# Performance work log

Hardware: AMD Instinct MI355X
Metric: run time of the kernel (lower is better)

## Reference

```python
import jax, jax.numpy as jnp
from jax import lax
import numpy as np

N_LOOP, N_LAYER, FS = 2, 10, 2
RES_CH, DIL_CH, SKIP_CH, COND_DIM = 64, 128, 128, 80
DILATIONS = [2 ** i for i in range(N_LAYER)] * N_LOOP  # 20 layers
L = len(DILATIONS)
B, T = 4, 8192


def setup_inputs() -> dict:
    key = jax.random.key(0)
    ks = jax.random.split(key, 10)
    s = 0.05
    return {
        "x": jax.random.normal(ks[0], (B, RES_CH, T, 1), jnp.float32),
        "condition": jax.random.normal(ks[1], (B, COND_DIM, T, 1), jnp.float32),
        # stacked per-layer params (L layers)
        "conv_w": jax.random.normal(ks[2], (L, DIL_CH, RES_CH, FS), jnp.float32) * s,
        "conv_b": jax.random.normal(ks[3], (L, DIL_CH), jnp.float32) * s,
        "cond_w": jax.random.normal(ks[4], (L, DIL_CH, COND_DIM), jnp.float32) * s,
        "cond_b": jax.random.normal(ks[5], (L, DIL_CH), jnp.float32) * s,
        "res_w": jax.random.normal(ks[6], (L, RES_CH, DIL_CH // 2), jnp.float32) * s,
        "res_b": jax.random.normal(ks[7], (L, RES_CH), jnp.float32) * s,
        "skip_w": jax.random.normal(ks[8], (L, SKIP_CH, DIL_CH // 2), jnp.float32) * s,
        "skip_b": jax.random.normal(ks[9], (L, SKIP_CH), jnp.float32) * s,
    }


def reference(x, condition, conv_w, conv_b, cond_w, cond_b, res_w, res_b, skip_w, skip_b):
    # Drop trailing width-1 dim: [B,C,T,1] -> [B,C,T]
    xs = x[..., 0]
    cond = condition[..., 0]
    skip_total = None
    for i, d in enumerate(DILATIONS):
        # torch pads d*(FS-1) on both sides then crops [:T] == left-only causal pad
        h = lax.conv_general_dilated(
            xs, conv_w[i], window_strides=(1,),
            padding=[(d * (FS - 1), 0)], rhs_dilation=(d,),
            dimension_numbers=("NCH", "OIH", "NCH"),
        ) + conv_b[i][None, :, None]
        # 1x1 condition projection, broadcast add
        h = h + jnp.einsum("ch,bht->bct", cond_w[i], cond) + cond_b[i][None, :, None]
        tanh_z, sig_z = jnp.split(h, 2, axis=1)
        z = jnp.tanh(tanh_z) * jax.nn.sigmoid(sig_z)  # [B, DIL_CH//2, T]
        xs = jnp.einsum("oc,bct->bot", res_w[i], z) + res_b[i][None, :, None] + xs
        skip = jnp.einsum("oc,bct->bot", skip_w[i], z) + skip_b[i][None, :, None]
        skip_total = skip if skip_total is None else skip_total + skip
    return skip_total[..., None]  # [B, SKIP_CH, T, 1]
```

## Files before the change

### kernel.cpp

```cpp
#include <hip/hip_runtime.h>

#define BATCH 4
#define TLEN 8192
#define NLAYER 20
#define NTILE 128
#define GUARD 8
#define ATILE (NTILE + GUARD)
#define CELL 4096

typedef __attribute__((ext_vector_type(8))) short bf16x8;
typedef __attribute__((ext_vector_type(8))) unsigned short u16x8;
typedef __attribute__((ext_vector_type(4))) short s16x4;
typedef __attribute__((ext_vector_type(4))) float f32x4;

__device__ __forceinline__ unsigned short f2b(float f) {
    unsigned u = __float_as_uint(f);
    return (unsigned short)((u + 0x7fffu + ((u >> 16) & 1u)) >> 16);
}
__device__ __forceinline__ unsigned cvtpk(float lo, float hi) {
    unsigned r;
    asm("v_cvt_pk_bf16_f32 %0, %1, %2" : "=v"(r) : "v"(lo), "v"(hi));
    return r;
}

__global__ void prep_w(const float* __restrict__ conv_w, const float* __restrict__ conv_b,
                       const float* __restrict__ cond_w, const float* __restrict__ cond_b,
                       const float* __restrict__ res_w,  const float* __restrict__ res_b,
                       const float* __restrict__ skip_w, const float* __restrict__ skip_b,
                       unsigned short* __restrict__ w1f, unsigned short* __restrict__ w2f,
                       unsigned short* __restrict__ wsf,
                       float* __restrict__ hb, float* __restrict__ rb, float* __restrict__ sbt) {
    const int l = blockIdx.x, tid = threadIdx.x;
    const int start = blockIdx.y * 256 + tid;
    for (int idx = start; idx < 7 * 8 * 512; idx += 2048) {
        int ks = idx >> 12;
        int slot = (idx >> 9) & 7, lane = (idx >> 3) & 63, j = idx & 7;
        int m = (slot & 1) * 64 + (slot >> 1) * 16 + (lane & 15);
        int k = ks * 32 + ((lane >> 4) << 3) + j;
        float v;
        if (k < 64)       v = conv_w[(((size_t)l * 128 + m) * 64 + k) * 2 + 0];
        else if (k < 128) v = conv_w[(((size_t)l * 128 + m) * 64 + (k - 64)) * 2 + 1];
        else if (k < 208) v = cond_w[((size_t)l * 128 + m) * 80 + (k - 128)];
        else              v = 0.0f;
        w1f[(size_t)l * 7 * 8 * 512 + idx] = f2b(v);
    }
    for (int idx = start; idx < 2 * 4 * 512; idx += 2048) {
        int ks = idx >> 11;
        int slot = (idx >> 9) & 3, lane = (idx >> 3) & 63, j = idx & 7;
        int m = slot * 16 + (lane & 15);
        int k = ks * 32 + ((lane >> 4) << 3) + j;
        w2f[(size_t)l * 2 * 4 * 512 + idx] = f2b(res_w[((size_t)l * 64 + m) * 64 + k]);
    }
    for (int idx = start; idx < 2 * 8 * 512; idx += 2048) {
        int ks = idx >> 12;
        int slot = (idx >> 9) & 7, lane = (idx >> 3) & 63, j = idx & 7;
        int m = slot * 16 + (lane & 15);
        int k = ks * 32 + ((lane >> 4) << 3) + j;
        wsf[(size_t)l * 2 * 8 * 512 + idx] = f2b(skip_w[((size_t)l * 128 + m) * 64 + k]);
    }
    if (blockIdx.y == 0) {
        if (tid < 128) hb[l * 128 + tid] = conv_b[l * 128 + tid] + cond_b[l * 128 + tid];
        if (tid < 64)  rb[l * 64 + tid] = res_b[l * 64 + tid];
        if (l == 0 && tid < 128) {
            float s = 0.f;
            for (int q = 0; q < NLAYER; ++q) s += skip_b[q * 128 + tid];
            sbt[tid] = s;
        }
    }
}

__global__ void prep_xc(const float* __restrict__ x, const float* __restrict__ cond,
                        unsigned short* __restrict__ xall, unsigned short* __restrict__ condc,
                        unsigned* __restrict__ flags) {
    const int tile = blockIdx.x, b = blockIdx.y, tid = threadIdx.x;
    if (tile < GUARD) {
        s16x4 zh = {0, 0, 0, 0};
        for (int s = 0; s < NLAYER; ++s) {
            unsigned short* g = xall + ((size_t)s * BATCH + b) * ATILE * CELL + (size_t)tile * CELL;
            for (int idx = tid * 4; idx < CELL; idx += 1024)
                *(s16x4*)(g + idx) = zh;
        }
        if (tile == 0)
            for (int i = tid; i < NTILE * 32; i += 256)
                flags[(size_t)b * NTILE * 32 + i] = 0u;
        return;
    }
    __shared__ float xt[64][64];
    __shared__ float ct[80][64];
    const int rt = tile - GUARD;
    for (int idx = tid; idx < 64 * 64; idx += 256) {
        int ch = idx >> 6, n = idx & 63;
        xt[ch][n] = x[((size_t)b * 64 + ch) * TLEN + rt * 64 + n];
    }
    for (int idx = tid; idx < 80 * 64; idx += 256) {
        int ch = idx >> 6, n = idx & 63;
        ct[ch][n] = cond[((size_t)b * 80 + ch) * TLEN + rt * 64 + n];
    }
    __syncthreads();
    unsigned short* s0 = xall + ((size_t)b * ATILE + tile) * CELL;
    for (int idx = tid; idx < 8 * 64; idx += 256) {
        int cg = idx >> 6, n = idx & 63;
        unsigned short* dbf = s0 + ((size_t)cg * 64 + n) * 8;
        #pragma unroll
        for (int j = 0; j < 8; ++j) dbf[j] = f2b(xt[cg * 8 + j][n]);
    }
    for (int idx = tid; idx < 12 * 64; idx += 256) {
        int cg = idx >> 6, n = idx & 63;
        u16x8 cell;
        #pragma unroll
        for (int j = 0; j < 8; ++j) {
            int ch = cg * 8 + j;
            cell[j] = (ch < 80) ? f2b(ct[ch][n]) : (unsigned short)0;
        }
        *(u16x8*)(condc + (((size_t)(b * NTILE + rt) * 12 + cg) * 64 + n) * 8) = cell;
    }
}

__global__ __launch_bounds__(256, 2) void wavenet_fused(
    const float* __restrict__ x, const unsigned short* __restrict__ condc,
    unsigned short* __restrict__ xall,
    const unsigned short* __restrict__ w1f, const unsigned short* __restrict__ w2f,
    const unsigned short* __restrict__ wsf,
    const float* __restrict__ hb, const float* __restrict__ rb,
    const float* __restrict__ sbt, float* __restrict__ out,
    unsigned* __restrict__ flags) {
    __shared__ unsigned short s_cond[12 * 512];
    __shared__ unsigned short s_xc[CELL];
    __shared__ unsigned short s_zc[CELL];

    const int b = blockIdx.y, tile = blockIdx.x, t0 = tile * 64;
    const int tid = threadIdx.x, lane = tid & 63;
    const int wv = __builtin_amdgcn_readfirstlane(tid >> 6);
    const int ln = lane & 15, lg = lane >> 4;
    const int r0 = wv * 16 + lg * 4;
    const int cgz = r0 >> 3, j0z = r0 & 7;
    const size_t bslot = (size_t)BATCH * ATILE * CELL;

    {
        const u16x8* cc = (const u16x8*)(condc + (size_t)(b * NTILE + tile) * 12 * 512);
        u16x8* sc = (u16x8*)s_cond;
        for (int i = tid; i < 768; i += 256) sc[i] = cc[i];
        const u16x8* xc = (const u16x8*)(xall + ((size_t)b * ATILE + tile + GUARD) * CELL);
        u16x8* sx = (u16x8*)s_xc;
        for (int i = tid; i < 512; i += 256) sx[i] = xc[i];
    }

    f32x4 xsr[4];
    #pragma unroll
    for (int nf = 0; nf < 4; ++nf)
        #pragma unroll
        for (int r = 0; r < 4; ++r)
            xsr[nf][r] = x[((size_t)b * 64 + r0 + r) * TLEN + t0 + nf * 16 + ln];

    f32x4 skacc[2][4];
    #pragma unroll
    for (int mf = 0; mf < 2; ++mf)
        #pragma unroll
        for (int nf = 0; nf < 4; ++nf) skacc[mf][nf] = (f32x4){0.f, 0.f, 0.f, 0.f};

    unsigned fc1 = 0, fc2 = 0, fc4 = 0, fc8 = 0;
    unsigned* myflag = flags + ((size_t)b * NTILE + tile) * 32 + wv;

    __syncthreads();

    for (int l = 0; l < NLAYER; ++l) {
        const int dil = 1 << ((l < 10) ? l : (l - 10));

        if (l > 0) {
            __syncthreads();
            const int kd = (dil + 63) >> 6;
            const int tp = tile - kd;
            if (tp >= 0) {
                unsigned cached = (kd == 1) ? fc1 : (kd == 2) ? fc2 : (kd == 4) ? fc4 : fc8;
                if (cached < (unsigned)l) {
                    const unsigned* fp = flags + ((size_t)b * NTILE + tp) * 32 + (lane & 3);
                    unsigned v;
                    for (;;) {
                        v = __hip_atomic_load(fp, __ATOMIC_RELAXED, __HIP_MEMORY_SCOPE_AGENT);
                        unsigned v1 = (unsigned)__shfl_xor((int)v, 1);
                        v = (v1 < v) ? v1 : v;
                        unsigned v2 = (unsigned)__shfl_xor((int)v, 2);
                        v = (v2 < v) ? v2 : v;
                        if (v >= (unsigned)l) break;
                        __builtin_amdgcn_s_sleep(2);
                    }
                    if (kd == 1) fc1 = v; else if (kd == 2) fc2 = v;
                    else if (kd == 4) fc4 = v; else fc8 = v;
                }
            }
            __builtin_amdgcn_sched_barrier(0);
        }

        const unsigned short* xrb = xall + (size_t)l * bslot + (size_t)b * ATILE * CELL;
        const unsigned short* w1l = w1f + (size_t)l * 7 * 8 * 512;

        bf16x8 brem[2][4];
        #pragma unroll
        for (int ks = 0; ks < 2; ++ks) {
            const int cg = ks * 4 + lg;
            #pragma unroll
            for (int nf = 0; nf < 4; ++nf) {
                int u = t0 + nf * 16 + ln - dil + GUARD * 64;
                brem[ks][nf] = *(const bf16x8*)(xrb + (((size_t)(u >> 6) * 8 + cg) * 64 + (u & 63)) * 8);
            }
        }
        bf16x8 raf[4];
        raf[0] = *(const bf16x8*)(w1l + (size_t)(0 * 8 + wv * 2 + 0) * 512 + lane * 8);
        raf[1] = *(const bf16x8*)(w1l + (size_t)(0 * 8 + wv * 2 + 1) * 512 + lane * 8);
        raf[2] = *(const bf16x8*)(w1l + (size_t)(1 * 8 + wv * 2 + 0) * 512 + lane * 8);
        raf[3] = *(const bf16x8*)(w1l + (size_t)(1 * 8 + wv * 2 + 1) * 512 + lane * 8);

        f32x4 acc[2][4];
        #pragma unroll
        for (int hf = 0; hf < 2; ++hf)
            #pragma unroll
            for (int nf = 0; nf < 4; ++nf) acc[hf][nf] = (f32x4){0.f, 0.f, 0.f, 0.f};

        #pragma unroll
        for (int ks = 2; ks < 7; ++ks) {
            bf16x8 af0 = *(const bf16x8*)(w1l + (size_t)(ks * 8 + wv * 2 + 0) * 512 + lane * 8);
            bf16x8 af1 = *(const bf16x8*)(w1l + (size_t)(ks * 8 + wv * 2 + 1) * 512 + lane * 8);
            bf16x8 bfr[4];
            if (ks < 4) {
                const int cg = (ks - 2) * 4 + lg;
                #pragma unroll
                for (int nf = 0; nf < 4; ++nf)
                    bfr[nf] = *(const bf16x8*)(s_xc + ((cg * 64) + nf * 16 + ln) * 8);
            } else {
                const int cg = (ks - 4) * 4 + lg;
                #pragma unroll
                for (int nf = 0; nf < 4; ++nf)
                    bfr[nf] = *(const bf16x8*)(s_cond + ((cg * 64) + nf * 16 + ln) * 8);
            }
            #pragma unroll
            for (int nf = 0; nf < 4; ++nf) {
                acc[0][nf] = __builtin_amdgcn_mfma_f32_16x16x32_bf16(af0, bfr[nf], acc[0][nf], 0, 0, 0);
                acc[1][nf] = __builtin_amdgcn_mfma_f32_16x16x32_bf16(af1, bfr[nf], acc[1][nf], 0, 0, 0);
            }
        }

        #pragma unroll
        for (int ks = 0; ks < 2; ++ks) {
            #pragma unroll
            for (int nf = 0; nf < 4; ++nf) {
                acc[0][nf] = __builtin_amdgcn_mfma_f32_16x16x32_bf16(raf[ks * 2 + 0], brem[ks][nf], acc[0][nf], 0, 0, 0);
                acc[1][nf] = __builtin_amdgcn_mfma_f32_16x16x32_bf16(raf[ks * 2 + 1], brem[ks][nf], acc[1][nf], 0, 0, 0);
            }
        }

        {
            const float* hbl = hb + l * 128;
            float4 hbt = *(const float4*)(hbl + r0);
            float4 hbs = *(const float4*)(hbl + 64 + r0);
            #pragma unroll
            for (int nf = 0; nf < 4; ++nf) {
                float zr[4];
                #pragma unroll
                for (int r = 0; r < 4; ++r) {
                    float a  = acc[0][nf][r] + ((r == 0) ? hbt.x : (r == 1) ? hbt.y : (r == 2) ? hbt.z : hbt.w);
                    float bs = acc[1][nf][r] + ((r == 0) ? hbs.x : (r == 1) ? hbs.y : (r == 2) ? hbs.z : hbs.w);
                    float e = __expf(a + a);
                    float s = __expf(-bs);
                    zr[r] = __fdividef(e - 1.0f, (e + 1.0f) * (1.0f + s));
                }
                union { unsigned u32[2]; s16x4 v; } pk;
                pk.u32[0] = cvtpk(zr[0], zr[1]);
                pk.u32[1] = cvtpk(zr[2], zr[3]);
                *(s16x4*)(&s_zc[((cgz * 64) + nf * 16 + ln) * 8 + j0z]) = pk.v;
            }
        }
        __syncthreads();

        bf16x8 bz[2][4];
        #pragma unroll
        for (int ks = 0; ks < 2; ++ks)
            #pragma unroll
            for (int nf = 0; nf < 4; ++nf)
                bz[ks][nf] = *(const bf16x8*)(&s_zc[(((ks * 4 + lg) * 64) + nf * 16 + ln) * 8]);
        const unsigned short* wsl = wsf + (size_t)l * 2 * 8 * 512;
        bf16x8 sw[2][2];
        #pragma unroll
        for (int ks = 0; ks < 2; ++ks) {
            sw[ks][0] = *(const bf16x8*)(wsl + (size_t)(ks * 8 + wv * 2 + 0) * 512 + lane * 8);
            sw[ks][1] = *(const bf16x8*)(wsl + (size_t)(ks * 8 + wv * 2 + 1) * 512 + lane * 8);
        }

        f32x4 acc2[4];
        #pragma unroll
        for (int nf = 0; nf < 4; ++nf) acc2[nf] = (f32x4){0.f, 0.f, 0.f, 0.f};
        const unsigned short* w2l = w2f + (size_t)l * 2 * 4 * 512;
        #pragma unroll
        for (int ks = 0; ks < 2; ++ks) {
            bf16x8 a2 = *(const bf16x8*)(w2l + (size_t)(ks * 4 + wv) * 512 + lane * 8);
            #pragma unroll
            for (int nf = 0; nf < 4; ++nf)
                acc2[nf] = __builtin_amdgcn_mfma_f32_16x16x32_bf16(a2, bz[ks][nf], acc2[nf], 0, 0, 0);
        }

        {
            const float* rbl = rb + l * 64;
            float4 rbv = *(const float4*)(rbl + r0);
            unsigned short* xwt = xall + (size_t)(l + 1) * bslot +
                                  ((size_t)b * ATILE + tile + GUARD) * CELL;
            #pragma unroll
            for (int nf = 0; nf < 4; ++nf) {
                xsr[nf][0] += acc2[nf][0] + rbv.x;
                xsr[nf][1] += acc2[nf][1] + rbv.y;
                xsr[nf][2] += acc2[nf][2] + rbv.z;
                xsr[nf][3] += acc2[nf][3] + rbv.w;
                if (l < NLAYER - 1) {
                    int n = nf * 16 + ln;
                    union { unsigned u32[2]; s16x4 v; unsigned long long u64; } pk;
                    pk.u32[0] = cvtpk(xsr[nf][0], xsr[nf][1]);
                    pk.u32[1] = cvtpk(xsr[nf][2], xsr[nf][3]);
                    *(s16x4*)(&s_xc[(cgz * 64 + n) * 8 + j0z]) = pk.v;
                    __hip_atomic_store((unsigned long long*)(xwt + ((size_t)cgz * 64 + n) * 8 + j0z),
                                       pk.u64, __ATOMIC_RELAXED, __HIP_MEMORY_SCOPE_AGENT);
                }
            }
        }

        #pragma unroll
        for (int ks = 0; ks < 2; ++ks)
            #pragma unroll
            for (int nf = 0; nf < 4; ++nf) {
                skacc[0][nf] = __builtin_amdgcn_mfma_f32_16x16x32_bf16(sw[ks][0], bz[ks][nf], skacc[0][nf], 0, 0, 0);
                skacc[1][nf] = __builtin_amdgcn_mfma_f32_16x16x32_bf16(sw[ks][1], bz[ks][nf], skacc[1][nf], 0, 0, 0);
            }

        if (l < NLAYER - 1) {
            asm volatile("s_waitcnt vmcnt(0)" ::: "memory");
            if (lane == 0)
                __hip_atomic_store(myflag, (unsigned)(l + 1),
                                   __ATOMIC_RELAXED, __HIP_MEMORY_SCOPE_AGENT);
        }
    }

    #pragma unroll
    for (int mf = 0; mf < 2; ++mf)
        #pragma unroll
        for (int nf = 0; nf < 4; ++nf)
            #pragma unroll
            for (int r = 0; r < 4; ++r) {
                int m = wv * 32 + mf * 16 + lg * 4 + r;
                out[((size_t)b * 128 + m) * TLEN + t0 + nf * 16 + ln] =
                    skacc[mf][nf][r] + sbt[m];
            }
}

extern "C" void kernel_launch(void* const* d_in, const int* in_sizes, int n_in,
                              void* d_out, int out_size, void* d_ws, size_t ws_size,
                              hipStream_t stream) {
    const float* x      = (const float*)d_in[0];
    const float* cond   = (const float*)d_in[1];
    const float* conv_w = (const float*)d_in[2];
    const float* conv_b = (const float*)d_in[3];
    const float* cond_w = (const float*)d_in[4];
    const float* cond_b = (const float*)d_in[5];
    const float* res_w  = (const float*)d_in[6];
    const float* res_b  = (const float*)d_in[7];
    const float* skip_w = (const float*)d_in[8];
    const float* skip_b = (const float*)d_in[9];
    float* out = (float*)d_out;

    char* ws = (char*)d_ws;
    const size_t XALL  = (size_t)NLAYER * BATCH * ATILE * CELL * 2;
    const size_t COND  = (size_t)BATCH * NTILE * 12 * 512 * 2;
    const size_t W1    = (size_t)NLAYER * 7 * 8 * 512 * 2;
    const size_t W2    = (size_t)NLAYER * 2 * 4 * 512 * 2;
    const size_t WSF   = (size_t)NLAYER * 2 * 8 * 512 * 2;
    const size_t HB    = NLAYER * 128 * 4;
    const size_t RB    = NLAYER * 64 * 4;
    const size_t SBT   = 256 * 4;
    const size_t FLAGS = (size_t)BATCH * NTILE * 32 * 4;

    size_t off = 0;
    unsigned short* xall  = (unsigned short*)(ws + off); off += XALL;
    unsigned short* condc = (unsigned short*)(ws + off); off += COND;
    unsigned short* w1f   = (unsigned short*)(ws + off); off += W1;
    unsigned short* w2f   = (unsigned short*)(ws + off); off += W2;
    unsigned short* wsf   = (unsigned short*)(ws + off); off += WSF;
    float* hb  = (float*)(ws + off); off += HB;
    float* rb  = (float*)(ws + off); off += RB;
    float* sbt = (float*)(ws + off); off += SBT;
    unsigned* flags = (unsigned*)(ws + off); off += FLAGS;

    prep_w<<<dim3(NLAYER, 8), 256, 0, stream>>>(conv_w, conv_b, cond_w, cond_b,
                                                res_w, res_b, skip_w, skip_b,
                                                w1f, w2f, wsf, hb, rb, sbt);
    prep_xc<<<dim3(ATILE, BATCH), 256, 0, stream>>>(x, cond, xall, condc, flags);

    wavenet_fused<<<dim3(NTILE, BATCH), 256, 0, stream>>>(
        x, condc, xall, w1f, w2f, wsf, hb, rb, sbt, out, flags);
}
```

Baseline: 128.0 us.

## Merge prep kernels and precompute next layer's condition GEMM before waiting on flags

Merges the weight-prep and input-prep kernels into a single launch, removing one kernel launch and its serialization. In the fused kernel, the condition-projection part of the layer-(l+1) gate GEMM (k-slices 4..6) no longer runs at the start of that layer. It now runs right after layer l publishes its flag and before the next layer's barrier and inter-tile flag spin, so this independent MFMA work can hide the dependency wait. The cost is that the accumulators stay live across the layer boundary, which adds register pressure.

```diff
diff --git a/kernel.cpp b/kernel.cpp
--- a/kernel.cpp
+++ b/kernel.cpp
@@ -23,56 +23,63 @@
     return r;
 }
 
-__global__ void prep_w(const float* __restrict__ conv_w, const float* __restrict__ conv_b,
-                       const float* __restrict__ cond_w, const float* __restrict__ cond_b,
-                       const float* __restrict__ res_w,  const float* __restrict__ res_b,
-                       const float* __restrict__ skip_w, const float* __restrict__ skip_b,
-                       unsigned short* __restrict__ w1f, unsigned short* __restrict__ w2f,
-                       unsigned short* __restrict__ wsf,
-                       float* __restrict__ hb, float* __restrict__ rb, float* __restrict__ sbt) {
-    const int l = blockIdx.x, tid = threadIdx.x;
-    const int start = blockIdx.y * 256 + tid;
-    for (int idx = start; idx < 7 * 8 * 512; idx += 2048) {
-        int ks = idx >> 12;
-        int slot = (idx >> 9) & 7, lane = (idx >> 3) & 63, j = idx & 7;
-        int m = (slot & 1) * 64 + (slot >> 1) * 16 + (lane & 15);
-        int k = ks * 32 + ((lane >> 4) << 3) + j;
-        float v;
-        if (k < 64)       v = conv_w[(((size_t)l * 128 + m) * 64 + k) * 2 + 0];
-        else if (k < 128) v = conv_w[(((size_t)l * 128 + m) * 64 + (k - 64)) * 2 + 1];
-        else if (k < 208) v = cond_w[((size_t)l * 128 + m) * 80 + (k - 128)];
-        else              v = 0.0f;
-        w1f[(size_t)l * 7 * 8 * 512 + idx] = f2b(v);
-    }
-    for (int idx = start; idx < 2 * 4 * 512; idx += 2048) {
-        int ks = idx >> 11;
-        int slot = (idx >> 9) & 3, lane = (idx >> 3) & 63, j = idx & 7;
-        int m = slot * 16 + (lane & 15);
-        int k = ks * 32 + ((lane >> 4) << 3) + j;
-        w2f[(size_t)l * 2 * 4 * 512 + idx] = f2b(res_w[((size_t)l * 64 + m) * 64 + k]);
-    }
-    for (int idx = start; idx < 2 * 8 * 512; idx += 2048) {
-        int ks = idx >> 12;
-        int slot = (idx >> 9) & 7, lane = (idx >> 3) & 63, j = idx & 7;
-        int m = slot * 16 + (lane & 15);
-        int k = ks * 32 + ((lane >> 4) << 3) + j;
-        wsf[(size_t)l * 2 * 8 * 512 + idx] = f2b(skip_w[((size_t)l * 128 + m) * 64 + k]);
-    }
-    if (blockIdx.y == 0) {
-        if (tid < 128) hb[l * 128 + tid] = conv_b[l * 128 + tid] + cond_b[l * 128 + tid];
-        if (tid < 64)  rb[l * 64 + tid] = res_b[l * 64 + tid];
-        if (l == 0 && tid < 128) {
-            float s = 0.f;
-            for (int q = 0; q < NLAYER; ++q) s += skip_b[q * 128 + tid];
-            sbt[tid] = s;
-        }
-    }
-}
-
-__global__ void prep_xc(const float* __restrict__ x, const float* __restrict__ cond,
-                        unsigned short* __restrict__ xall, unsigned short* __restrict__ condc,
-                        unsigned* __restrict__ flags) {
-    const int tile = blockIdx.x, b = blockIdx.y, tid = threadIdx.x;
+__global__ void prep_all(const float* __restrict__ x, const float* __restrict__ cond,
+                         const float* __restrict__ conv_w, const float* __restrict__ conv_b,
+                         const float* __restrict__ cond_w, const float* __restrict__ cond_b,
+                         const float* __restrict__ res_w,  const float* __restrict__ res_b,
+                         const float* __restrict__ skip_w, const float* __restrict__ skip_b,
+                         unsigned short* __restrict__ w1f, unsigned short* __restrict__ w2f,
+                         unsigned short* __restrict__ wsf, float* __restrict__ hb,
+                         float* __restrict__ rb, float* __restrict__ sbt,
+                         unsigned short* __restrict__ xall, unsigned short* __restrict__ condc,
+                         unsigned* __restrict__ flags) {
+    __shared__ float xt[64][64];
+    __shared__ float ct[80][64];
+    const int bid = blockIdx.x, tid = threadIdx.x;
+
+    if (bid < NLAYER * 8) {
+        const int l = bid >> 3;
+        const int start = (bid & 7) * 256 + tid;
+        for (int idx = start; idx < 7 * 8 * 512; idx += 2048) {
+            int ks = idx >> 12;
+            int slot = (idx >> 9) & 7, lane = (idx >> 3) & 63, j = idx & 7;
+            int m = (slot & 1) * 64 + (slot >> 1) * 16 + (lane & 15);
+            int k = ks * 32 + ((lane >> 4) << 3) + j;
+            float v;
+            if (k < 64)       v = conv_w[(((size_t)l * 128 + m) * 64 + k) * 2 + 0];
+            else if (k < 128) v = conv_w[(((size_t)l * 128 + m) * 64 + (k - 64)) * 2 + 1];
+            else if (k < 208) v = cond_w[((size_t)l * 128 + m) * 80 + (k - 128)];
+            else              v = 0.0f;
+            w1f[(size_t)l * 7 * 8 * 512 + idx] = f2b(v);
+        }
+        for (int idx = start; idx < 2 * 4 * 512; idx += 2048) {
+            int ks = idx >> 11;
+            int slot = (idx >> 9) & 3, lane = (idx >> 3) & 63, j = idx & 7;
+            int m = slot * 16 + (lane & 15);
+            int k = ks * 32 + ((lane >> 4) << 3) + j;
+            w2f[(size_t)l * 2 * 4 * 512 + idx] = f2b(res_w[((size_t)l * 64 + m) * 64 + k]);
+        }
+        for (int idx = start; idx < 2 * 8 * 512; idx += 2048) {
+            int ks = idx >> 12;
+            int slot = (idx >> 9) & 7, lane = (idx >> 3) & 63, j = idx & 7;
+            int m = slot * 16 + (lane & 15);
+            int k = ks * 32 + ((lane >> 4) << 3) + j;
+            wsf[(size_t)l * 2 * 8 * 512 + idx] = f2b(skip_w[((size_t)l * 128 + m) * 64 + k]);
+        }
+        if ((bid & 7) == 0) {
+            if (tid < 128) hb[l * 128 + tid] = conv_b[l * 128 + tid] + cond_b[l * 128 + tid];
+            if (tid < 64)  rb[l * 64 + tid] = res_b[l * 64 + tid];
+            if (l == 0 && tid < 128) {
+                float s = 0.f;
+                for (int q = 0; q < NLAYER; ++q) s += skip_b[q * 128 + tid];
+                sbt[tid] = s;
+            }
+        }
+        return;
+    }
+
+    const int r = bid - NLAYER * 8;
+    const int tile = r % ATILE, b = r / ATILE;
     if (tile < GUARD) {
         s16x4 zh = {0, 0, 0, 0};
         for (int s = 0; s < NLAYER; ++s) {
@@ -85,8 +92,6 @@
                 flags[(size_t)b * NTILE * 32 + i] = 0u;
         return;
     }
-    __shared__ float xt[64][64];
-    __shared__ float ct[80][64];
     const int rt = tile - GUARD;
     for (int idx = tid; idx < 64 * 64; idx += 256) {
         int ch = idx >> 6, n = idx & 63;
@@ -162,6 +167,28 @@
     unsigned* myflag = flags + ((size_t)b * NTILE + tile) * 32 + wv;
 
     __syncthreads();
+
+    f32x4 acc[2][4];
+
+    {
+        const unsigned short* w10 = w1f;
+        #pragma unroll
+        for (int hf = 0; hf < 2; ++hf)
+            #pragma unroll
+            for (int nf = 0; nf < 4; ++nf) acc[hf][nf] = (f32x4){0.f, 0.f, 0.f, 0.f};
+        #pragma unroll
+        for (int ks = 4; ks < 7; ++ks) {
+            bf16x8 af0 = *(const bf16x8*)(w10 + (size_t)(ks * 8 + wv * 2 + 0) * 512 + lane * 8);
+            bf16x8 af1 = *(const bf16x8*)(w10 + (size_t)(ks * 8 + wv * 2 + 1) * 512 + lane * 8);
+            const int cg = (ks - 4) * 4 + lg;
+            #pragma unroll
+            for (int nf = 0; nf < 4; ++nf) {
+                bf16x8 bfr = *(const bf16x8*)(s_cond + ((cg * 64) + nf * 16 + ln) * 8);
+                acc[0][nf] = __builtin_amdgcn_mfma_f32_16x16x32_bf16(af0, bfr, acc[0][nf], 0, 0, 0);
+                acc[1][nf] = __builtin_amdgcn_mfma_f32_16x16x32_bf16(af1, bfr, acc[1][nf], 0, 0, 0);
+            }
+        }
+    }
 
     for (int l = 0; l < NLAYER; ++l) {
         const int dil = 1 << ((l < 10) ? l : (l - 10));
@@ -210,32 +237,16 @@
         raf[2] = *(const bf16x8*)(w1l + (size_t)(1 * 8 + wv * 2 + 0) * 512 + lane * 8);
         raf[3] = *(const bf16x8*)(w1l + (size_t)(1 * 8 + wv * 2 + 1) * 512 + lane * 8);
 
-        f32x4 acc[2][4];
-        #pragma unroll
-        for (int hf = 0; hf < 2; ++hf)
-            #pragma unroll
-            for (int nf = 0; nf < 4; ++nf) acc[hf][nf] = (f32x4){0.f, 0.f, 0.f, 0.f};
-
-        #pragma unroll
-        for (int ks = 2; ks < 7; ++ks) {
+        #pragma unroll
+        for (int ks = 2; ks < 4; ++ks) {
             bf16x8 af0 = *(const bf16x8*)(w1l + (size_t)(ks * 8 + wv * 2 + 0) * 512 + lane * 8);
             bf16x8 af1 = *(const bf16x8*)(w1l + (size_t)(ks * 8 + wv * 2 + 1) * 512 + lane * 8);
-            bf16x8 bfr[4];
-            if (ks < 4) {
-                const int cg = (ks - 2) * 4 + lg;
-                #pragma unroll
-                for (int nf = 0; nf < 4; ++nf)
-                    bfr[nf] = *(const bf16x8*)(s_xc + ((cg * 64) + nf * 16 + ln) * 8);
-            } else {
-                const int cg = (ks - 4) * 4 + lg;
-                #pragma unroll
-                for (int nf = 0; nf < 4; ++nf)
-                    bfr[nf] = *(const bf16x8*)(s_cond + ((cg * 64) + nf * 16 + ln) * 8);
-            }
-            #pragma unroll
-            for (int nf = 0; nf < 4; ++nf) {
-                acc[0][nf] = __builtin_amdgcn_mfma_f32_16x16x32_bf16(af0, bfr[nf], acc[0][nf], 0, 0, 0);
-                acc[1][nf] = __builtin_amdgcn_mfma_f32_16x16x32_bf16(af1, bfr[nf], acc[1][nf], 0, 0, 0);
+            const int cg = (ks - 2) * 4 + lg;
+            #pragma unroll
+            for (int nf = 0; nf < 4; ++nf) {
+                bf16x8 bfr = *(const bf16x8*)(s_xc + ((cg * 64) + nf * 16 + ln) * 8);
+                acc[0][nf] = __builtin_amdgcn_mfma_f32_16x16x32_bf16(af0, bfr, acc[0][nf], 0, 0, 0);
+                acc[1][nf] = __builtin_amdgcn_mfma_f32_16x16x32_bf16(af1, bfr, acc[1][nf], 0, 0, 0);
             }
         }
 
@@ -333,6 +344,26 @@
             if (lane == 0)
                 __hip_atomic_store(myflag, (unsigned)(l + 1),
                                    __ATOMIC_RELAXED, __HIP_MEMORY_SCOPE_AGENT);
+        }
+
+        if (l < NLAYER - 1) {
+            const unsigned short* w1n = w1f + (size_t)(l + 1) * 7 * 8 * 512;
+            #pragma unroll
+            for (int hf = 0; hf < 2; ++hf)
+                #pragma unroll
+                for (int nf = 0; nf < 4; ++nf) acc[hf][nf] = (f32x4){0.f, 0.f, 0.f, 0.f};
+            #pragma unroll
+            for (int ks = 4; ks < 7; ++ks) {
+                bf16x8 af0 = *(const bf16x8*)(w1n + (size_t)(ks * 8 + wv * 2 + 0) * 512 + lane * 8);
+                bf16x8 af1 = *(const bf16x8*)(w1n + (size_t)(ks * 8 + wv * 2 + 1) * 512 + lane * 8);
+                const int cg = (ks - 4) * 4 + lg;
+                #pragma unroll
+                for (int nf = 0; nf < 4; ++nf) {
+                    bf16x8 bfr = *(const bf16x8*)(s_cond + ((cg * 64) + nf * 16 + ln) * 8);
+                    acc[0][nf] = __builtin_amdgcn_mfma_f32_16x16x32_bf16(af0, bfr, acc[0][nf], 0, 0, 0);
+                    acc[1][nf] = __builtin_amdgcn_mfma_f32_16x16x32_bf16(af1, bfr, acc[1][nf], 0, 0, 0);
+                }
+            }
         }
     }
 
@@ -385,10 +416,9 @@
     float* sbt = (float*)(ws + off); off += SBT;
     unsigned* flags = (unsigned*)(ws + off); off += FLAGS;
 
-    prep_w<<<dim3(NLAYER, 8), 256, 0, stream>>>(conv_w, conv_b, cond_w, cond_b,
-                                                res_w, res_b, skip_w, skip_b,
-                                                w1f, w2f, wsf, hb, rb, sbt);
-    prep_xc<<<dim3(ATILE, BATCH), 256, 0, stream>>>(x, cond, xall, condc, flags);
+    prep_all<<<NLAYER * 8 + ATILE * BATCH, 256, 0, stream>>>(
+        x, cond, conv_w, conv_b, cond_w, cond_b, res_w, res_b, skip_w, skip_b,
+        w1f, w2f, wsf, hb, rb, sbt, xall, condc, flags);
 
     wavenet_fused<<<dim3(NTILE, BATCH), 256, 0, stream>>>(
         x, condc, xall, w1f, w2f, wsf, hb, rb, sbt, out, flags);
```

Result: faster. 118.2 us (median of 2 runs) (-7.7%).
